# Kernel tuning notes

Hardware: AMD Instinct MI355X
Metric: run time of the kernel (lower is better)

## Reference

```python
import jax, jax.numpy as jnp
import numpy as np


def setup_inputs() -> dict:
    key = jax.random.key(0)
    k1, k2 = jax.random.split(key)
    B, N, M, D = 8, 8192, 8192, 3
    pred_seq = jax.random.normal(k1, (B, N, D), dtype=jnp.float32)
    tgt_output = jax.random.normal(k2, (B, M, D), dtype=jnp.float32)
    return {"pred_seq": pred_seq, "tgt_output": tgt_output}


def reference(pred_seq, tgt_output):
    # Euclidean pairwise distances [B, N, M] (== torch.cdist with p=2).
    # The torch module computes both cdist(pred,tgt) and cdist(tgt,pred);
    # they are transposes, so we compute one matrix and min over both axes.
    sq_p = jnp.sum(pred_seq * pred_seq, axis=-1)      # [B, N]
    sq_t = jnp.sum(tgt_output * tgt_output, axis=-1)  # [B, M]
    cross = jnp.einsum('bnd,bmd->bnm', pred_seq, tgt_output)  # [B, N, M]
    d2 = sq_p[:, :, None] + sq_t[:, None, :] - 2.0 * cross
    d = jnp.sqrt(jnp.maximum(d2, 0.0))
    min_pred_to_true = jnp.min(d, axis=2)   # [B, N]
    min_true_to_pred = jnp.min(d, axis=1)   # [B, M]
    chamfer = (jnp.mean(min_pred_to_true, axis=1) + jnp.mean(min_true_to_pred, axis=1)) / 2.0
    return chamfer  # [B]
```

## Files before the change

### kernel.cpp

```cpp
#include <hip/hip_runtime.h>
#include <math.h>

#define BB 8
#define NN 8192
#define MM 8192
#define BN (BB * NN)
#define BM (BB * MM)

#define BLOCK 256
#define RROWS 8
#define QB (BLOCK * RROWS)
#define SPLIT 64

#define INF_KEY 0x7F7F7F7F

__device__ __forceinline__ int enc_key(float v) {
    int b = __float_as_int(v);
    return b >= 0 ? b : (b ^ 0x7fffffff);
}
__device__ __forceinline__ float dec_key(int k) {
    int b = k >= 0 ? k : (k ^ 0x7fffffff);
    return __int_as_float(b);
}

__global__ __launch_bounds__(BLOCK) void chamfer_pack(
        const float* __restrict__ pred, const float* __restrict__ tgt,
        float4* __restrict__ pp, float4* __restrict__ pt,
        int* __restrict__ rk, int* __restrict__ ck,
        float* __restrict__ out) {
    int i = blockIdx.x * BLOCK + threadIdx.x;
    {
        float x = pred[i * 3 + 0], y = pred[i * 3 + 1], z = pred[i * 3 + 2];
        pp[i] = make_float4(x, y, z, fmaf(x, x, fmaf(y, y, z * z)));
    }
    {
        float x = tgt[i * 3 + 0], y = tgt[i * 3 + 1], z = tgt[i * 3 + 2];
        pt[i] = make_float4(x, y, z, fmaf(x, x, fmaf(y, y, z * z)));
    }
    rk[i] = INF_KEY;
    ck[i] = INF_KEY;
    if (blockIdx.x == 0 && threadIdx.x < BB) out[threadIdx.x] = 0.0f;
}

__global__ __launch_bounds__(BLOCK) void chamfer_minpass(
        const float4* __restrict__ pp, const float4* __restrict__ pt,
        int* __restrict__ rk, int* __restrict__ ck) {
    const bool second = (blockIdx.z != 0);
    const float4* __restrict__ qry = second ? pt : pp;
    const float4* __restrict__ tgt = second ? pp : pt;
    int* __restrict__ okeys = second ? ck : rk;

    const int qbase = blockIdx.x * QB;
    const int b = qbase / NN;
    const int t = threadIdx.x;

    float nx[RROWS], ny[RROWS], nz[RROWS], rmin[RROWS];
    #pragma unroll
    for (int r = 0; r < RROWS; ++r) {
        float4 p = qry[qbase + r * BLOCK + t];
        nx[r] = -2.0f * p.x;
        ny[r] = -2.0f * p.y;
        nz[r] = -2.0f * p.z;
        rmin[r] = INFINITY;
    }

    const int mc = MM / SPLIT;
    const float4* __restrict__ tp = tgt + (size_t)b * MM + (size_t)blockIdx.y * mc;

#define PROC(tt)                                          \
    {                                                     \
        _Pragma("unroll")                                 \
        for (int r = 0; r < RROWS; ++r) {                 \
            float v = fmaf(nx[r], (tt).x, (tt).w);        \
            v = fmaf(ny[r], (tt).y, v);                   \
            v = fmaf(nz[r], (tt).z, v);                   \
            rmin[r] = fminf(rmin[r], v);                  \
        }                                                 \
    }

    float4 c0 = tp[0], c1 = tp[1], c2 = tp[2], c3 = tp[3];
    #pragma unroll 1
    for (int m = 0; m + 8 <= mc; m += 4) {
        float4 n0 = tp[m + 4], n1 = tp[m + 5], n2 = tp[m + 6], n3 = tp[m + 7];
        PROC(c0); PROC(c1); PROC(c2); PROC(c3);
        c0 = n0; c1 = n1; c2 = n2; c3 = n3;
    }
    PROC(c0); PROC(c1); PROC(c2); PROC(c3);
#undef PROC

    #pragma unroll
    for (int r = 0; r < RROWS; ++r)
        atomicMin(&okeys[qbase + r * BLOCK + t], enc_key(rmin[r]));
}

#define FSLICE 8
__global__ __launch_bounds__(BLOCK) void chamfer_finalize(
        const int* __restrict__ rk, const int* __restrict__ ck,
        const float4* __restrict__ pp, const float4* __restrict__ pt,
        float* __restrict__ out) {
    const int b = blockIdx.x / FSLICE;
    const int s = blockIdx.x % FSLICE;
    const int t = threadIdx.x;
    const int span = NN / FSLICE;
    float sA = 0.0f, sB = 0.0f;
    for (int n = s * span + t; n < (s + 1) * span; n += BLOCK) {
        int i = b * NN + n;
        float d2 = pp[i].w + dec_key(rk[i]);
        sA += sqrtf(fmaxf(d2, 0.0f));
    }
    for (int m = s * span + t; m < (s + 1) * span; m += BLOCK) {
        int i = b * MM + m;
        float d2 = pt[i].w + dec_key(ck[i]);
        sB += sqrtf(fmaxf(d2, 0.0f));
    }
    __shared__ float red[BLOCK];
    red[t] = 0.5f * (sA / (float)NN + sB / (float)MM);
    __syncthreads();
    for (int off = BLOCK / 2; off > 0; off >>= 1) {
        if (t < off) red[t] += red[t + off];
        __syncthreads();
    }
    if (t == 0) atomicAdd(&out[b], red[0]);
}

extern "C" void kernel_launch(void* const* d_in, const int* in_sizes, int n_in,
                              void* d_out, int out_size, void* d_ws, size_t ws_size,
                              hipStream_t stream) {
    const float* pred = (const float*)d_in[0];
    const float* tgtp = (const float*)d_in[1];
    float* out = (float*)d_out;

    char* ws = (char*)d_ws;
    float4* pp = (float4*)ws;
    float4* pt = (float4*)(ws + (size_t)BN * sizeof(float4));
    int* rk = (int*)(ws + (size_t)(BN + BM) * sizeof(float4));
    int* ck = rk + BN;

    chamfer_pack<<<BN / BLOCK, BLOCK, 0, stream>>>(pred, tgtp, pp, pt, rk, ck, out);

    chamfer_minpass<<<dim3(BN / QB, SPLIT, 2), BLOCK, 0, stream>>>(pp, pt, rk, ck);

    chamfer_finalize<<<BB * FSLICE, BLOCK, 0, stream>>>(rk, ck, pp, pt, out);
}
```

Baseline: 155.8 us.

## Pack points in pairs and use packed fp32 FMA in min pass

Changes the packed point layout to pair two points as SoA (x0,x1,y0,y1 / z0,z1,w0,w1) and rewrites the inner distance loop to use 2-wide vector FMAs, evaluating two target points per instruction. This targets VALU throughput, since MI355X offers packed FP32 FMA. The pack and finalize kernels are adapted to the new layout, and the manual software prefetch is replaced by a plain unrolled loop. It relies on the compiler emitting v_pk_fma_f32, and the extra fminf per pair adds some instructions.

```diff
diff --git a/kernel.cpp b/kernel.cpp
--- a/kernel.cpp
+++ b/kernel.cpp
@@ -6,6 +6,7 @@
 #define MM 8192
 #define BN (BB * NN)
 #define BM (BB * MM)
+#define NPAIR (BN / 2)
 
 #define BLOCK 256
 #define RROWS 8
@@ -13,6 +14,8 @@
 #define SPLIT 64
 
 #define INF_KEY 0x7F7F7F7F
+
+typedef float v2f __attribute__((ext_vector_type(2)));
 
 __device__ __forceinline__ int enc_key(float v) {
     int b = __float_as_int(v);
@@ -28,17 +31,25 @@
         float4* __restrict__ pp, float4* __restrict__ pt,
         int* __restrict__ rk, int* __restrict__ ck,
         float* __restrict__ out) {
-    int i = blockIdx.x * BLOCK + threadIdx.x;
+    int j = blockIdx.x * BLOCK + threadIdx.x;
     {
-        float x = pred[i * 3 + 0], y = pred[i * 3 + 1], z = pred[i * 3 + 2];
-        pp[i] = make_float4(x, y, z, fmaf(x, x, fmaf(y, y, z * z)));
+        const float* p = pred + (size_t)j * 6;
+        float x0 = p[0], y0 = p[1], z0 = p[2], x1 = p[3], y1 = p[4], z1 = p[5];
+        float w0 = fmaf(x0, x0, fmaf(y0, y0, z0 * z0));
+        float w1 = fmaf(x1, x1, fmaf(y1, y1, z1 * z1));
+        pp[j * 2 + 0] = make_float4(x0, x1, y0, y1);
+        pp[j * 2 + 1] = make_float4(z0, z1, w0, w1);
     }
     {
-        float x = tgt[i * 3 + 0], y = tgt[i * 3 + 1], z = tgt[i * 3 + 2];
-        pt[i] = make_float4(x, y, z, fmaf(x, x, fmaf(y, y, z * z)));
+        const float* p = tgt + (size_t)j * 6;
+        float x0 = p[0], y0 = p[1], z0 = p[2], x1 = p[3], y1 = p[4], z1 = p[5];
+        float w0 = fmaf(x0, x0, fmaf(y0, y0, z0 * z0));
+        float w1 = fmaf(x1, x1, fmaf(y1, y1, z1 * z1));
+        pt[j * 2 + 0] = make_float4(x0, x1, y0, y1);
+        pt[j * 2 + 1] = make_float4(z0, z1, w0, w1);
     }
-    rk[i] = INF_KEY;
-    ck[i] = INF_KEY;
+    ((int2*)rk)[j] = make_int2(INF_KEY, INF_KEY);
+    ((int2*)ck)[j] = make_int2(INF_KEY, INF_KEY);
     if (blockIdx.x == 0 && threadIdx.x < BB) out[threadIdx.x] = 0.0f;
 }
 
@@ -54,39 +65,41 @@
     const int b = qbase / NN;
     const int t = threadIdx.x;
 
-    float nx[RROWS], ny[RROWS], nz[RROWS], rmin[RROWS];
+    v2f nxp[RROWS], nyp[RROWS], nzp[RROWS];
+    float rmin[RROWS];
     #pragma unroll
     for (int r = 0; r < RROWS; ++r) {
-        float4 p = qry[qbase + r * BLOCK + t];
-        nx[r] = -2.0f * p.x;
-        ny[r] = -2.0f * p.y;
-        nz[r] = -2.0f * p.z;
+        int i = qbase + r * BLOCK + t;
+        float4 A = qry[(i >> 1) * 2 + 0];
+        float4 Bq = qry[(i >> 1) * 2 + 1];
+        float x = (i & 1) ? A.y : A.x;
+        float y = (i & 1) ? A.w : A.z;
+        float z = (i & 1) ? Bq.y : Bq.x;
+        nxp[r] = (v2f){-2.0f * x, -2.0f * x};
+        nyp[r] = (v2f){-2.0f * y, -2.0f * y};
+        nzp[r] = (v2f){-2.0f * z, -2.0f * z};
         rmin[r] = INFINITY;
     }
 
     const int mc = MM / SPLIT;
-    const float4* __restrict__ tp = tgt + (size_t)b * MM + (size_t)blockIdx.y * mc;
+    const float4* __restrict__ tp4 = tgt + (size_t)b * MM + (size_t)blockIdx.y * mc;
 
-#define PROC(tt)                                          \
-    {                                                     \
-        _Pragma("unroll")                                 \
-        for (int r = 0; r < RROWS; ++r) {                 \
-            float v = fmaf(nx[r], (tt).x, (tt).w);        \
-            v = fmaf(ny[r], (tt).y, v);                   \
-            v = fmaf(nz[r], (tt).z, v);                   \
-            rmin[r] = fminf(rmin[r], v);                  \
-        }                                                 \
+    #pragma unroll 4
+    for (int jp = 0; jp < mc / 2; ++jp) {
+        float4 A = tp4[jp * 2 + 0];
+        float4 Bt = tp4[jp * 2 + 1];
+        v2f xx = (v2f){A.x, A.y};
+        v2f yy = (v2f){A.z, A.w};
+        v2f zz = (v2f){Bt.x, Bt.y};
+        v2f ww = (v2f){Bt.z, Bt.w};
+        #pragma unroll
+        for (int r = 0; r < RROWS; ++r) {
+            v2f acc = __builtin_elementwise_fma(nxp[r], xx, ww);
+            acc = __builtin_elementwise_fma(nyp[r], yy, acc);
+            acc = __builtin_elementwise_fma(nzp[r], zz, acc);
+            rmin[r] = fminf(rmin[r], fminf(acc[0], acc[1]));
+        }
     }
-
-    float4 c0 = tp[0], c1 = tp[1], c2 = tp[2], c3 = tp[3];
-    #pragma unroll 1
-    for (int m = 0; m + 8 <= mc; m += 4) {
-        float4 n0 = tp[m + 4], n1 = tp[m + 5], n2 = tp[m + 6], n3 = tp[m + 7];
-        PROC(c0); PROC(c1); PROC(c2); PROC(c3);
-        c0 = n0; c1 = n1; c2 = n2; c3 = n3;
-    }
-    PROC(c0); PROC(c1); PROC(c2); PROC(c3);
-#undef PROC
 
     #pragma unroll
     for (int r = 0; r < RROWS; ++r)
@@ -102,15 +115,19 @@
     const int s = blockIdx.x % FSLICE;
     const int t = threadIdx.x;
     const int span = NN / FSLICE;
+    const float* ppf = (const float*)pp;
+    const float* ptf = (const float*)pt;
     float sA = 0.0f, sB = 0.0f;
     for (int n = s * span + t; n < (s + 1) * span; n += BLOCK) {
         int i = b * NN + n;
-        float d2 = pp[i].w + dec_key(rk[i]);
+        float w = ppf[(size_t)(i >> 1) * 8 + 6 + (i & 1)];
+        float d2 = w + dec_key(rk[i]);
         sA += sqrtf(fmaxf(d2, 0.0f));
     }
     for (int m = s * span + t; m < (s + 1) * span; m += BLOCK) {
         int i = b * MM + m;
-        float d2 = pt[i].w + dec_key(ck[i]);
+        float w = ptf[(size_t)(i >> 1) * 8 + 6 + (i & 1)];
+        float d2 = w + dec_key(ck[i]);
         sB += sqrtf(fmaxf(d2, 0.0f));
     }
     __shared__ float red[BLOCK];
@@ -136,7 +153,7 @@
     int* rk = (int*)(ws + (size_t)(BN + BM) * sizeof(float4));
     int* ck = rk + BN;
 
-    chamfer_pack<<<BN / BLOCK, BLOCK, 0, stream>>>(pred, tgtp, pp, pt, rk, ck, out);
+    chamfer_pack<<<NPAIR / BLOCK, BLOCK, 0, stream>>>(pred, tgtp, pp, pt, rk, ck, out);
 
     chamfer_minpass<<<dim3(BN / QB, SPLIT, 2), BLOCK, 0, stream>>>(pp, pt, rk, ck);
 
```

Result: faster. 144.5 us (-7.3%).
